# Kernel optimization log

Hardware: AMD Instinct MI355X
Metric: run time of the kernel (lower is better)

The kernel has to match this reference:

```python
import jax, jax.numpy as jnp
import numpy as np

ROI_BATCHSIZE = 512
FG_PER_IMAGE = 128  # round(0.25 * 512)
FG_THRESH = 0.5
BG_HI = 0.5
BG_LO = 0.0


def _make_boxes(key, b, n, img=1024.0):
    k1, k2 = jax.random.split(key)
    xy = jax.random.uniform(k1, (b, n, 2), minval=0.0, maxval=img - 300.0)
    wh = jax.random.uniform(k2, (b, n, 2), minval=8.0, maxval=300.0)
    return jnp.concatenate([xy, xy + wh], axis=-1)  # [b, n, 4] valid x1y1x2y2


def setup_inputs() -> dict:
    key = jax.random.key(0)
    B, R, G = 16, 20000, 100
    k1, k2, k3 = jax.random.split(key, 3)
    roi_boxes = _make_boxes(k1, B, R)
    all_rois = jnp.concatenate([jnp.zeros((B, R, 1), jnp.float32), roi_boxes], axis=-1)
    gt_b = _make_boxes(k2, B, G)
    gt_lab = jax.random.randint(k3, (B, G, 1), 1, 21).astype(jnp.float32)
    gt_boxes = jnp.concatenate([gt_b, gt_lab], axis=-1)
    return {
        "all_rois": all_rois,
        "gt_boxes": gt_boxes,
        "bbox_means": jnp.zeros((4,), jnp.float32),
        "bbox_stds": jnp.array([0.1, 0.1, 0.2, 0.2], jnp.float32),
        "num_gt_boxes": jnp.full((B,), G, jnp.int32),
    }


def _pairwise_iou(a, b):  # a: [B,N,4], b: [B,G,4] -> [B,N,G]
    area_a = (a[..., 2] - a[..., 0] + 1.0) * (a[..., 3] - a[..., 1] + 1.0)
    area_b = (b[..., 2] - b[..., 0] + 1.0) * (b[..., 3] - b[..., 1] + 1.0)
    iw = jnp.clip(jnp.minimum(a[:, :, None, 2], b[:, None, :, 2])
                  - jnp.maximum(a[:, :, None, 0], b[:, None, :, 0]) + 1.0, 0.0)
    ih = jnp.clip(jnp.minimum(a[:, :, None, 3], b[:, None, :, 3])
                  - jnp.maximum(a[:, :, None, 1], b[:, None, :, 1]) + 1.0, 0.0)
    inter = iw * ih
    return inter / (area_a[:, :, None] + area_b[:, None, :] - inter)


def _encode(ex, gt):  # [B,S,4] each -> [B,S,4] (dx, dy, dw, dh)
    ew = ex[..., 2] - ex[..., 0] + 1.0
    eh = ex[..., 3] - ex[..., 1] + 1.0
    ecx = ex[..., 0] + 0.5 * ew
    ecy = ex[..., 1] + 0.5 * eh
    gw = gt[..., 2] - gt[..., 0] + 1.0
    gh = gt[..., 3] - gt[..., 1] + 1.0
    gcx = gt[..., 0] + 0.5 * gw
    gcy = gt[..., 1] + 0.5 * gh
    return jnp.stack([(gcx - ecx) / ew, (gcy - ecy) / eh,
                      jnp.log(gw / ew), jnp.log(gh / eh)], axis=-1)


def _sample_one(key, max_ov, labels_i, rois_i, gta_i, gt_i, img_idx):
    # max_ov: [N]; rois_i: [N,5]; gta_i: [N]; gt_i: [G,5]
    N = max_ov.shape[0]
    S = ROI_BATCHSIZE
    k1, k2, k3, k4 = jax.random.split(key, 4)
    fg = max_ov >= FG_THRESH
    bg = (max_ov < BG_HI) & (max_ov >= BG_LO)
    nfg = fg.sum()
    nbg = bg.sum()
    # random permutation of fg (bg) candidates packed to the front
    fg_order = jnp.argsort(jnp.where(fg, jax.random.uniform(k1, (N,)), 2.0))
    bg_order = jnp.argsort(jnp.where(bg, jax.random.uniform(k2, (N,)), 2.0))
    n_fg_take = jnp.where(nbg > 0, jnp.minimum(FG_PER_IMAGE, nfg), S)
    n_fg_take = jnp.where(nfg > 0, n_fg_take, 0)
    slots = jnp.arange(S)
    rf = jax.random.uniform(k3, (S,))
    rb = jax.random.uniform(k4, (S,))
    # fg without replacement (main path) or with replacement (no-bg path)
    fg_wr = fg_order[jnp.clip((rf * nfg.astype(rf.dtype)).astype(jnp.int32), 0, N - 1)]
    fg_pick = jnp.where(nbg > 0, fg_order[jnp.minimum(slots, N - 1)], fg_wr)
    # bg always sampled with replacement, as in the original
    bg_pick = bg_order[jnp.clip((rb * nbg.astype(rb.dtype)).astype(jnp.int32), 0, N - 1)]
    keep = jnp.where(slots < n_fg_take, fg_pick, bg_pick)  # [S]
    labels = jnp.where(slots < n_fg_take, labels_i[keep], 0.0)
    rois = rois_i[keep].at[:, 0].set(img_idx)
    gt_rois = gt_i[gta_i[keep]]  # [S,5]
    return rois, labels, gt_rois


def _forward(all_rois, gt_boxes, bbox_means, bbox_stds):
    B, G = gt_boxes.shape[0], gt_boxes.shape[1]
    # append gt boxes as rois (col 0 zeroed, cols 1:5 = gt box)
    gt_append = jnp.concatenate(
        [jnp.zeros_like(gt_boxes[..., :1]), gt_boxes[..., :4]], axis=-1)
    all_rois = jnp.concatenate([all_rois, gt_append], axis=1)  # [B, R+G, 5]
    overlaps = _pairwise_iou(all_rois[..., 1:5], gt_boxes[..., :4])  # [B,N,G]
    max_ov = overlaps.max(axis=2)
    gt_assign = overlaps.argmax(axis=2)
    labels = jnp.take_along_axis(gt_boxes[..., 4], gt_assign, axis=1)  # [B,N]
    keys = jax.random.split(jax.random.key(42), B)
    rois_b, labels_b, gt_rois_b = jax.vmap(_sample_one)(
        keys, max_ov, labels, all_rois, gt_assign, gt_boxes,
        jnp.arange(B, dtype=all_rois.dtype))
    targets = _encode(rois_b[..., 1:5], gt_rois_b[..., :4])
    targets = (targets - bbox_means) / bbox_stds
    targets = targets * (labels_b > 0).astype(targets.dtype)[..., None]
    return rois_b, labels_b, targets


def reference(all_rois, gt_boxes, bbox_means, bbox_stds, num_gt_boxes):
    # num_gt_boxes is accepted but unused, as in the original forward
    return _forward(all_rois, gt_boxes, bbox_means, bbox_stds)
```

## Files before the change

kernel.cpp:

```cpp
#include <hip/hip_runtime.h>
#include <stdint.h>


typedef uint32_t u32;
typedef uint64_t u64;

constexpr int B    = 16;
constexpr int R    = 20000;
constexpr int G    = 100;
constexpr int N    = R + G;
constexpr int S    = 512;
constexpr int KFG  = 128;
constexpr int NBKT = 8192;
constexpr u32 SENT = 0xFFFFFFFFu;
constexpr int TPB  = 256;
constexpr int NBLK = (N + TPB - 1) / TPB;

__device__ __forceinline__ void tf2x32(u32 k0, u32 k1, u32 x0, u32 x1,
                                       u32& o0, u32& o1) {
  u32 ks2 = k0 ^ k1 ^ 0x1BD11BDAu;
#define TFR(r) { x0 += x1; x1 = (x1 << (r)) | (x1 >> (32 - (r))); x1 ^= x0; }
  x0 += k0; x1 += k1;
  TFR(13) TFR(15) TFR(26) TFR(6)
  x0 += k1;  x1 += ks2 + 1u;
  TFR(17) TFR(29) TFR(16) TFR(24)
  x0 += ks2; x1 += k0 + 2u;
  TFR(13) TFR(15) TFR(26) TFR(6)
  x0 += k0;  x1 += k1 + 3u;
  TFR(17) TFR(29) TFR(16) TFR(24)
  x0 += k1;  x1 += ks2 + 4u;
  TFR(13) TFR(15) TFR(26) TFR(6)
  x0 += ks2; x1 += k0 + 5u;
#undef TFR
  o0 = x0; o1 = x1;
}

__device__ __forceinline__ void batch_key(int b, u32& kb0, u32& kb1) {
  tf2x32(0u, 42u, 0u, (u32)b, kb0, kb1);
}
__device__ __forceinline__ void sub_key(u32 kb0, u32 kb1, int j, u32& k0, u32& k1) {
  tf2x32(kb0, kb1, 0u, (u32)j, k0, k1);
}
__device__ __forceinline__ u32 rand_bits(u32 k0, u32 k1, int i) {
  u32 b0, b1;
  tf2x32(k0, k1, 0u, (u32)i, b0, b1);
  return b0 ^ b1;
}
__device__ __forceinline__ float bits_to_uniform(u32 bits) {
  return __uint_as_float((bits >> 9) | 0x3f800000u) - 1.0f;
}

__global__ __launch_bounds__(256) void k_zero(uint4* __restrict__ p) {
  const int i = blockIdx.x * 256 + threadIdx.x;
  p[i] = make_uint4(0u, 0u, 0u, 0u);
}

__global__ __launch_bounds__(TPB) void
k_mask(const float* __restrict__ rois, const float* __restrict__ gts,
       u32* __restrict__ fgkey, u32* __restrict__ bgkey,
       u32* __restrict__ cnt,
       u32* __restrict__ minblkF, u32* __restrict__ minblkB) {
#pragma clang fp contract(off)
  __shared__ float4 gbox[G];
  __shared__ float garea[G];
  __shared__ u32 wminF[TPB / 64], wminB[TPB / 64];
  const int b = blockIdx.y;
  if (threadIdx.x < G) {
    const float* gp = gts + (size_t)(b * G + threadIdx.x) * 5;
    float x1 = gp[0], y1 = gp[1], x2 = gp[2], y2 = gp[3];
    gbox[threadIdx.x] = make_float4(x1, y1, x2, y2);
    garea[threadIdx.x] = (x2 - x1 + 1.0f) * (y2 - y1 + 1.0f);
  }
  __syncthreads();

  const int n = blockIdx.x * TPB + threadIdx.x;
  const bool valid = n < N;
  const int nl = valid ? n : 0;

  float ax1, ay1, ax2, ay2;
  if (nl < R) {
    const float* rp = rois + (size_t)(b * R + nl) * 5;
    ax1 = rp[1]; ay1 = rp[2]; ax2 = rp[3]; ay2 = rp[4];
  } else {
    const float* gp = gts + (size_t)(b * G + (nl - R)) * 5;
    ax1 = gp[0]; ay1 = gp[1]; ax2 = gp[2]; ay2 = gp[3];
  }
  const float areaa = (ax2 - ax1 + 1.0f) * (ay2 - ay1 + 1.0f);

  int fg = 0;
#pragma unroll 4
  for (int g = 0; g < G; ++g) {
    const float4 gb = gbox[g];
    const float gar = garea[g];
    float iw = fminf(ax2, gb.z) - fmaxf(ax1, gb.x) + 1.0f;
    iw = fmaxf(iw, 0.0f);
    float ih = fminf(ay2, gb.w) - fmaxf(ay1, gb.y) + 1.0f;
    ih = fmaxf(ih, 0.0f);
    float inter = iw * ih;
    float denom = (areaa + gar) - inter;
    fg |= ((double)inter >= (double)denom * 0x1.ffffffp-2);
  }

  u32 kb0, kb1, k10, k11, k20, k21;
  batch_key(b, kb0, kb1);
  sub_key(kb0, kb1, 0, k10, k11);
  sub_key(kb0, kb1, 1, k20, k21);
  if (valid) {
    u32 u1 = rand_bits(k10, k11, n) >> 9;
    u32 u2 = rand_bits(k20, k21, n) >> 9;
    fgkey[(size_t)b * N + n] = fg ? u1 : SENT;
    bgkey[(size_t)b * N + n] = fg ? SENT : u2;
    const u32 uk = fg ? u1 : u2;
    const int set = fg ? 0 : 1;
    atomicAdd((unsigned int*)&cnt[((size_t)b * 2 + set) * NBKT + (uk >> 10)], 1u);
  }

  u32 vF = (valid && !fg) ? (u32)n : SENT;
  u32 vB = (valid &&  fg) ? (u32)n : SENT;
#pragma unroll
  for (int m = 1; m <= 32; m <<= 1) {
    vF = min(vF, (u32)__shfl_xor((int)vF, m));
    vB = min(vB, (u32)__shfl_xor((int)vB, m));
  }
  if ((threadIdx.x & 63) == 0) {
    wminF[threadIdx.x >> 6] = vF;
    wminB[threadIdx.x >> 6] = vB;
  }
  __syncthreads();
  if (threadIdx.x == 0) {
    u32 mF = SENT, mB = SENT;
#pragma unroll
    for (int w = 0; w < TPB / 64; ++w) { mF = min(mF, wminF[w]); mB = min(mB, wminB[w]); }
    minblkF[b * NBLK + blockIdx.x] = mF;
    minblkB[b * NBLK + blockIdx.x] = mB;
  }
}

__global__ __launch_bounds__(1024) void
k_scan(u32* __restrict__ cnt, u32* __restrict__ cur,
       int* __restrict__ nfg, int* __restrict__ nbg,
       const u32* __restrict__ minblkF, const u32* __restrict__ minblkB,
       u32* __restrict__ slotF, u32* __restrict__ slotB) {
  constexpr int T = 1024;
  constexpr int PER = NBKT / T;
  __shared__ u32 sh[T];
  const int b = blockIdx.x, set = blockIdx.y;
  const int tid = threadIdx.x;
  u32* c = cnt + ((size_t)b * 2 + set) * NBKT;
  u32* q = cur + ((size_t)b * 2 + set) * NBKT;
  u32 local[PER];
  u32 tot = 0;
  const int base = tid * PER;
#pragma unroll
  for (int i = 0; i < PER; ++i) { u32 v = c[base + i]; local[i] = tot; tot += v; }
  sh[tid] = tot;
  __syncthreads();
  for (int off = 1; off < T; off <<= 1) {
    u32 v = (tid >= off) ? sh[tid - off] : 0u;
    __syncthreads();
    sh[tid] += v;
    __syncthreads();
  }
  const u32 pre = sh[tid] - tot;
  const u32 total = sh[T - 1];
#pragma unroll
  for (int i = 0; i < PER; ++i) { u32 v = pre + local[i]; c[base + i] = v; q[base + i] = v; }

  if (tid < 64) {
    const u32* mb = (set ? minblkB : minblkF) + b * NBLK;
    u32 m = SENT;
    for (int i = tid; i < NBLK; i += 64) m = min(m, mb[i]);
#pragma unroll
    for (int mm = 1; mm <= 32; mm <<= 1) m = min(m, (u32)__shfl_xor((int)m, mm));
    if (tid == 0) {
      u32* slot = (set ? slotB : slotF) + (size_t)b * N;
      if (total < (u32)N) slot[total] = (m == SENT) ? 0u : m;
      if (set) nbg[b] = (int)total; else nfg[b] = (int)total;
    }
  }
}

__global__ void k_scatter(const u32* __restrict__ fgkey, const u32* __restrict__ bgkey,
                          u32* __restrict__ cur,
                          u32* __restrict__ slotF, u32* __restrict__ slotB) {
  const int b = blockIdx.y;
  const int n = blockIdx.x * blockDim.x + threadIdx.x;
  if (n >= N) return;
  u32 kf = fgkey[(size_t)b * N + n];
  if (kf != SENT) {
    u32 pos = atomicAdd((unsigned int*)&cur[((size_t)b * 2 + 0) * NBKT + (kf >> 10)], 1u);
    slotF[(size_t)b * N + pos] = ((kf & 1023u) << 15) | (u32)n;
  }
  u32 kb = bgkey[(size_t)b * N + n];
  if (kb != SENT) {
    u32 pos = atomicAdd((unsigned int*)&cur[((size_t)b * 2 + 1) * NBKT + (kb >> 10)], 1u);
    slotB[(size_t)b * N + pos] = ((kb & 1023u) << 15) | (u32)n;
  }
}

__global__ void k_bsort(const u32* __restrict__ cnt ,
                        const u32* __restrict__ cur ,
                        u32* __restrict__ slotF, u32* __restrict__ slotB) {
  const int t = blockIdx.x * blockDim.x + threadIdx.x;
  const int total = B * 2 * NBKT;
  if (t >= total) return;
  const int bs = t / NBKT;
  u32* slot = ((bs & 1) ? slotB : slotF) + (size_t)(bs >> 1) * N;
  const u32 s0 = cnt[t];
  const u32 e = cur[t];
  for (u32 i = s0 + 1; i < e; ++i) {
    u32 v = slot[i];
    int j = (int)i - 1;
    while (j >= (int)s0 && slot[j] > v) { slot[j + 1] = slot[j]; --j; }
    slot[j + 1] = v;
  }
}

__global__ void k_sample(const float* __restrict__ rois, const float* __restrict__ gts,
                         const float* __restrict__ means, const float* __restrict__ stds,
                         const int* __restrict__ nfgA, const int* __restrict__ nbgA,
                         const u32* __restrict__ slotF, const u32* __restrict__ slotB,
                         float* __restrict__ out) {
#pragma clang fp contract(off)
  __shared__ float4 gbox[G];
  __shared__ float garea[G];
  __shared__ float glab[G];
  const int b = blockIdx.x;
  const int s = threadIdx.x;
  if (s < G) {
    const float* gp = gts + (size_t)(b * G + s) * 5;
    float x1 = gp[0], y1 = gp[1], x2 = gp[2], y2 = gp[3];
    gbox[s] = make_float4(x1, y1, x2, y2);
    garea[s] = (x2 - x1 + 1.0f) * (y2 - y1 + 1.0f);
    glab[s] = gp[4];
  }
  __syncthreads();

  const int nfg = nfgA[b];
  const int nbg = nbgA[b];

  u32 kb0, kb1, k30, k31, k40, k41;
  batch_key(b, kb0, kb1);
  sub_key(kb0, kb1, 2, k30, k31);
  sub_key(kb0, kb1, 3, k40, k41);
  float rf = bits_to_uniform(rand_bits(k30, k31, s));
  float rb = bits_to_uniform(rand_bits(k40, k41, s));

  int n_fg_take = (nbg > 0) ? min(KFG, nfg) : S;
  if (nfg <= 0) n_fg_take = 0;

  int keep;
  if (s < n_fg_take) {
    int fi;
    if (nbg > 0) fi = s;
    else {
      fi = (int)(rf * (float)nfg);
      fi = max(0, min(fi, nfg));
    }
    keep = (int)(slotF[(size_t)b * N + fi] & 0x7FFFu);
  } else {
    if (nbg > 0) {
      int bi = (int)(rb * (float)nbg);
      bi = max(0, min(bi, nbg));
      keep = (int)(slotB[(size_t)b * N + bi] & 0x7FFFu);
    } else {
      keep = 0;
    }
  }
  keep = max(0, min(keep, N - 1));

  float ax1, ay1, ax2, ay2;
  if (keep < R) {
    const float* rp = rois + (size_t)(b * R + keep) * 5;
    ax1 = rp[1]; ay1 = rp[2]; ax2 = rp[3]; ay2 = rp[4];
  } else {
    const float4 g2 = gbox[keep - R];
    ax1 = g2.x; ay1 = g2.y; ax2 = g2.z; ay2 = g2.w;
  }
  const float areaa = (ax2 - ax1 + 1.0f) * (ay2 - ay1 + 1.0f);

  float best = -1.0f;
  int arg = 0;
  for (int g = 0; g < G; ++g) {
    const float4 gb = gbox[g];
    const float gar = garea[g];
    float iw = fminf(ax2, gb.z) - fmaxf(ax1, gb.x) + 1.0f;
    iw = fmaxf(iw, 0.0f);
    float ih = fminf(ay2, gb.w) - fmaxf(ay1, gb.y) + 1.0f;
    ih = fmaxf(ih, 0.0f);
    float inter = iw * ih;
    float denom = (areaa + gar) - inter;
    float iou = inter / denom;
    if (iou > best) { best = iou; arg = g; }
  }

  const bool isfg = s < n_fg_take;
  const float label = isfg ? glab[arg] : 0.0f;
  const float4 gbx = gbox[arg];
  const float gx1 = gbx.x, gy1 = gbx.y, gx2 = gbx.z, gy2 = gbx.w;

  float ew = ax2 - ax1 + 1.0f, eh = ay2 - ay1 + 1.0f;
  float ecx = ax1 + 0.5f * ew, ecy = ay1 + 0.5f * eh;
  float gw = gx2 - gx1 + 1.0f, gh = gy2 - gy1 + 1.0f;
  float gcx = gx1 + 0.5f * gw, gcy = gy1 + 0.5f * gh;
  float t0 = (gcx - ecx) / ew;
  float t1 = (gcy - ecy) / eh;
  float t2 = logf(gw / ew);
  float t3 = logf(gh / eh);
  const float msk = (label > 0.0f) ? 1.0f : 0.0f;
  t0 = (t0 - means[0]) / stds[0] * msk;
  t1 = (t1 - means[1]) / stds[1] * msk;
  t2 = (t2 - means[2]) / stds[2] * msk;
  t3 = (t3 - means[3]) / stds[3] * msk;

  float* rout = out;
  float* lout = out + (size_t)B * S * 5;
  float* tout = lout + (size_t)B * S;
  float* rp2 = rout + (size_t)(b * S + s) * 5;
  rp2[0] = (float)b;
  rp2[1] = ax1; rp2[2] = ay1; rp2[3] = ax2; rp2[4] = ay2;
  lout[b * S + s] = label;
  float* tp = tout + (size_t)(b * S + s) * 4;
  tp[0] = t0; tp[1] = t1; tp[2] = t2; tp[3] = t3;
}

extern "C" void kernel_launch(void* const* d_in, const int* in_sizes, int n_in,
                              void* d_out, int out_size, void* d_ws, size_t ws_size,
                              hipStream_t stream) {
  const float* rois  = (const float*)d_in[0];
  const float* gts   = (const float*)d_in[1];
  const float* means = (const float*)d_in[2];
  const float* stds  = (const float*)d_in[3];

  char* ws = (char*)d_ws;
  const size_t per = (size_t)B * N;
  const size_t bkts = (size_t)B * 2 * NBKT;
  u32* fgkey   = (u32*)ws; ws += per * sizeof(u32);
  u32* bgkey   = (u32*)ws; ws += per * sizeof(u32);
  u32* slotF   = (u32*)ws; ws += per * sizeof(u32);
  u32* slotB   = (u32*)ws; ws += per * sizeof(u32);
  u32* cnt     = (u32*)ws; ws += bkts * sizeof(u32);
  u32* cur     = (u32*)ws; ws += bkts * sizeof(u32);
  u32* minblkF = (u32*)ws; ws += (size_t)B * NBLK * sizeof(u32);
  u32* minblkB = (u32*)ws; ws += (size_t)B * NBLK * sizeof(u32);
  int* nfg     = (int*)ws; ws += B * sizeof(int);
  int* nbg     = (int*)ws; ws += B * sizeof(int);

  hipLaunchKernelGGL(k_zero, dim3((int)(bkts / 4 / 256)), dim3(256), 0, stream,
                     (uint4*)cnt);

  hipLaunchKernelGGL(k_mask, dim3(NBLK, B), dim3(TPB), 0, stream,
                     rois, gts, fgkey, bgkey, cnt, minblkF, minblkB);
  hipLaunchKernelGGL(k_scan, dim3(B, 2), dim3(1024), 0, stream,
                     cnt, cur, nfg, nbg, minblkF, minblkB, slotF, slotB);
  hipLaunchKernelGGL(k_scatter, dim3((N + 255) / 256, B), dim3(256), 0, stream,
                     fgkey, bgkey, cur, slotF, slotB);
  hipLaunchKernelGGL(k_bsort, dim3((B * 2 * NBKT + 255) / 256), dim3(256), 0, stream,
                     cnt, cur, slotF, slotB);
  hipLaunchKernelGGL(k_sample, dim3(B), dim3(S), 0, stream,
                     rois, gts, means, stds, nfg, nbg, slotF, slotB,
                     (float*)d_out);
}
```

Measured before the change: 82.35 us.

## Replace per-bucket insertion sort with on-demand rank selection in sampler

```diff
diff --git a/kernel.cpp b/kernel.cpp
--- a/kernel.cpp
+++ b/kernel.cpp
@@ -3,7 +3,6 @@
 
 
 typedef uint32_t u32;
-typedef uint64_t u64;
 
 constexpr int B    = 16;
 constexpr int R    = 20000;
@@ -11,7 +10,7 @@
 constexpr int N    = R + G;
 constexpr int S    = 512;
 constexpr int KFG  = 128;
-constexpr int NBKT = 8192;
+constexpr int NBKT = 2048;
 constexpr u32 SENT = 0xFFFFFFFFu;
 constexpr int TPB  = 256;
 constexpr int NBLK = (N + TPB - 1) / TPB;
@@ -51,14 +50,12 @@
 }
 
 __global__ __launch_bounds__(256) void k_zero(uint4* __restrict__ p) {
-  const int i = blockIdx.x * 256 + threadIdx.x;
-  p[i] = make_uint4(0u, 0u, 0u, 0u);
+  p[blockIdx.x * 256 + threadIdx.x] = make_uint4(0u, 0u, 0u, 0u);
 }
 
 __global__ __launch_bounds__(TPB) void
 k_mask(const float* __restrict__ rois, const float* __restrict__ gts,
-       u32* __restrict__ fgkey, u32* __restrict__ bgkey,
-       u32* __restrict__ cnt,
+       u32* __restrict__ ckey, u32* __restrict__ cnt,
        u32* __restrict__ minblkF, u32* __restrict__ minblkB) {
 #pragma clang fp contract(off)
   __shared__ float4 gbox[G];
@@ -106,13 +103,12 @@
   sub_key(kb0, kb1, 0, k10, k11);
   sub_key(kb0, kb1, 1, k20, k21);
   if (valid) {
-    u32 u1 = rand_bits(k10, k11, n) >> 9;
-    u32 u2 = rand_bits(k20, k21, n) >> 9;
-    fgkey[(size_t)b * N + n] = fg ? u1 : SENT;
-    bgkey[(size_t)b * N + n] = fg ? SENT : u2;
-    const u32 uk = fg ? u1 : u2;
-    const int set = fg ? 0 : 1;
-    atomicAdd((unsigned int*)&cnt[((size_t)b * 2 + set) * NBKT + (uk >> 10)], 1u);
+    u32 kk0 = fg ? k10 : k20;
+    u32 kk1 = fg ? k11 : k21;
+    u32 key = rand_bits(kk0, kk1, n) >> 9;
+    u32 set = fg ? 0u : 1u;
+    ckey[(size_t)b * N + n] = key | (set << 31);
+    atomicAdd((unsigned int*)&cnt[((size_t)b * 2 + set) * NBKT + (key >> 12)], 1u);
   }
 
   u32 vF = (valid && !fg) ? (u32)n : SENT;
@@ -136,103 +132,96 @@
   }
 }
 
-__global__ __launch_bounds__(1024) void
-k_scan(u32* __restrict__ cnt, u32* __restrict__ cur,
+__global__ __launch_bounds__(64) void
+k_scan(u32* __restrict__ cnt,
        int* __restrict__ nfg, int* __restrict__ nbg,
        const u32* __restrict__ minblkF, const u32* __restrict__ minblkB,
        u32* __restrict__ slotF, u32* __restrict__ slotB) {
-  constexpr int T = 1024;
-  constexpr int PER = NBKT / T;
-  __shared__ u32 sh[T];
+  constexpr int PER = NBKT / 64;
   const int b = blockIdx.x, set = blockIdx.y;
-  const int tid = threadIdx.x;
+  const int lane = threadIdx.x;
   u32* c = cnt + ((size_t)b * 2 + set) * NBKT;
-  u32* q = cur + ((size_t)b * 2 + set) * NBKT;
-  u32 local[PER];
+  u32 v[PER];
   u32 tot = 0;
-  const int base = tid * PER;
-#pragma unroll
-  for (int i = 0; i < PER; ++i) { u32 v = c[base + i]; local[i] = tot; tot += v; }
-  sh[tid] = tot;
-  __syncthreads();
-  for (int off = 1; off < T; off <<= 1) {
-    u32 v = (tid >= off) ? sh[tid - off] : 0u;
-    __syncthreads();
-    sh[tid] += v;
-    __syncthreads();
-  }
-  const u32 pre = sh[tid] - tot;
-  const u32 total = sh[T - 1];
-#pragma unroll
-  for (int i = 0; i < PER; ++i) { u32 v = pre + local[i]; c[base + i] = v; q[base + i] = v; }
-
-  if (tid < 64) {
-    const u32* mb = (set ? minblkB : minblkF) + b * NBLK;
-    u32 m = SENT;
-    for (int i = tid; i < NBLK; i += 64) m = min(m, mb[i]);
-#pragma unroll
-    for (int mm = 1; mm <= 32; mm <<= 1) m = min(m, (u32)__shfl_xor((int)m, mm));
-    if (tid == 0) {
-      u32* slot = (set ? slotB : slotF) + (size_t)b * N;
-      if (total < (u32)N) slot[total] = (m == SENT) ? 0u : m;
-      if (set) nbg[b] = (int)total; else nfg[b] = (int)total;
-    }
-  }
-}
-
-__global__ void k_scatter(const u32* __restrict__ fgkey, const u32* __restrict__ bgkey,
-                          u32* __restrict__ cur,
+  const int base = lane * PER;
+#pragma unroll
+  for (int i = 0; i < PER; ++i) { u32 t = c[base + i]; v[i] = tot; tot += t; }
+  u32 run = tot;
+#pragma unroll
+  for (int m = 1; m < 64; m <<= 1) {
+    u32 up = (u32)__shfl_up((int)run, m);
+    if (lane >= m) run += up;
+  }
+  const u32 pre = run - tot;
+  const u32 total = (u32)__shfl((int)run, 63);
+#pragma unroll
+  for (int i = 0; i < PER; ++i) c[base + i] = pre + v[i];
+
+  const u32* mb = (set ? minblkB : minblkF) + b * NBLK;
+  u32 m = SENT;
+  for (int i = lane; i < NBLK; i += 64) m = min(m, mb[i]);
+#pragma unroll
+  for (int mm = 1; mm <= 32; mm <<= 1) m = min(m, (u32)__shfl_xor((int)m, mm));
+  if (lane == 0) {
+    u32* slot = (set ? slotB : slotF) + (size_t)b * N;
+    if (total < (u32)N) slot[total] = (m == SENT) ? 0u : m;
+    if (set) nbg[b] = (int)total; else nfg[b] = (int)total;
+  }
+}
+
+__global__ void k_scatter(const u32* __restrict__ ckey, u32* __restrict__ cnt,
                           u32* __restrict__ slotF, u32* __restrict__ slotB) {
   const int b = blockIdx.y;
   const int n = blockIdx.x * blockDim.x + threadIdx.x;
   if (n >= N) return;
-  u32 kf = fgkey[(size_t)b * N + n];
-  if (kf != SENT) {
-    u32 pos = atomicAdd((unsigned int*)&cur[((size_t)b * 2 + 0) * NBKT + (kf >> 10)], 1u);
-    slotF[(size_t)b * N + pos] = ((kf & 1023u) << 15) | (u32)n;
-  }
-  u32 kb = bgkey[(size_t)b * N + n];
-  if (kb != SENT) {
-    u32 pos = atomicAdd((unsigned int*)&cur[((size_t)b * 2 + 1) * NBKT + (kb >> 10)], 1u);
-    slotB[(size_t)b * N + pos] = ((kb & 1023u) << 15) | (u32)n;
-  }
-}
-
-__global__ void k_bsort(const u32* __restrict__ cnt ,
-                        const u32* __restrict__ cur ,
-                        u32* __restrict__ slotF, u32* __restrict__ slotB) {
-  const int t = blockIdx.x * blockDim.x + threadIdx.x;
-  const int total = B * 2 * NBKT;
-  if (t >= total) return;
-  const int bs = t / NBKT;
-  u32* slot = ((bs & 1) ? slotB : slotF) + (size_t)(bs >> 1) * N;
-  const u32 s0 = cnt[t];
-  const u32 e = cur[t];
-  for (u32 i = s0 + 1; i < e; ++i) {
-    u32 v = slot[i];
-    int j = (int)i - 1;
-    while (j >= (int)s0 && slot[j] > v) { slot[j + 1] = slot[j]; --j; }
-    slot[j + 1] = v;
-  }
-}
-
-__global__ void k_sample(const float* __restrict__ rois, const float* __restrict__ gts,
-                         const float* __restrict__ means, const float* __restrict__ stds,
-                         const int* __restrict__ nfgA, const int* __restrict__ nbgA,
-                         const u32* __restrict__ slotF, const u32* __restrict__ slotB,
-                         float* __restrict__ out) {
+  const u32 w = ckey[(size_t)b * N + n];
+  const u32 set = w >> 31;
+  const u32 key = w & 0x7FFFFFu;
+  u32 pos = atomicAdd((unsigned int*)&cnt[((size_t)b * 2 + set) * NBKT + (key >> 12)], 1u);
+  u32* slot = (set ? slotB : slotF) + (size_t)b * N;
+  slot[pos] = ((key & 4095u) << 15) | (u32)n;
+}
+
+__device__ __forceinline__ int pick_rank(const u32* __restrict__ cend,
+                                         const u32* __restrict__ slot,
+                                         int r, int total) {
+  if (r >= total) return (int)(slot[total] & 0x7FFFu);
+  int lo = 0, hi = NBKT - 1;
+  while (lo < hi) {
+    int mid = (lo + hi) >> 1;
+    if (cend[mid] > (u32)r) hi = mid; else lo = mid + 1;
+  }
+  const u32 bs = lo ? cend[lo - 1] : 0u;
+  const u32 k = cend[lo] - bs;
+  const u32 target = (u32)r - bs;
+  for (u32 i = 0; i < k; ++i) {
+    u32 e = slot[bs + i];
+    u32 rk = 0;
+    for (u32 j = 0; j < k; ++j) rk += (slot[bs + j] < e);
+    if (rk == target) return (int)(e & 0x7FFFu);
+  }
+  return 0;
+}
+
+__global__ __launch_bounds__(128) void
+k_sample(const float* __restrict__ rois, const float* __restrict__ gts,
+         const float* __restrict__ means, const float* __restrict__ stds,
+         const int* __restrict__ nfgA, const int* __restrict__ nbgA,
+         const u32* __restrict__ cnt,
+         const u32* __restrict__ slotF, const u32* __restrict__ slotB,
+         float* __restrict__ out) {
 #pragma clang fp contract(off)
   __shared__ float4 gbox[G];
   __shared__ float garea[G];
   __shared__ float glab[G];
   const int b = blockIdx.x;
-  const int s = threadIdx.x;
-  if (s < G) {
-    const float* gp = gts + (size_t)(b * G + s) * 5;
+  const int s = blockIdx.y * 128 + threadIdx.x;
+  if (threadIdx.x < G) {
+    const float* gp = gts + (size_t)(b * G + threadIdx.x) * 5;
     float x1 = gp[0], y1 = gp[1], x2 = gp[2], y2 = gp[3];
-    gbox[s] = make_float4(x1, y1, x2, y2);
-    garea[s] = (x2 - x1 + 1.0f) * (y2 - y1 + 1.0f);
-    glab[s] = gp[4];
+    gbox[threadIdx.x] = make_float4(x1, y1, x2, y2);
+    garea[threadIdx.x] = (x2 - x1 + 1.0f) * (y2 - y1 + 1.0f);
+    glab[threadIdx.x] = gp[4];
   }
   __syncthreads();
 
@@ -249,23 +238,26 @@
   int n_fg_take = (nbg > 0) ? min(KFG, nfg) : S;
   if (nfg <= 0) n_fg_take = 0;
 
+  const u32* cF = cnt + ((size_t)b * 2 + 0) * NBKT;
+  const u32* cB = cnt + ((size_t)b * 2 + 1) * NBKT;
+  const u32* sF = slotF + (size_t)b * N;
+  const u32* sB = slotB + (size_t)b * N;
+
   int keep;
   if (s < n_fg_take) {
     int fi;
     if (nbg > 0) fi = s;
     else {
       fi = (int)(rf * (float)nfg);
-      fi = max(0, min(fi, nfg));
+      fi = max(0, min(fi, N - 1));
     }
-    keep = (int)(slotF[(size_t)b * N + fi] & 0x7FFFu);
+    keep = pick_rank(cF, sF, fi, nfg);
+  } else if (nbg > 0) {
+    int bi = (int)(rb * (float)nbg);
+    bi = max(0, min(bi, N - 1));
+    keep = pick_rank(cB, sB, bi, nbg);
   } else {
-    if (nbg > 0) {
-      int bi = (int)(rb * (float)nbg);
-      bi = max(0, min(bi, nbg));
-      keep = (int)(slotB[(size_t)b * N + bi] & 0x7FFFu);
-    } else {
-      keep = 0;
-    }
+    keep = 0;
   }
   keep = max(0, min(keep, N - 1));
 
@@ -335,12 +327,10 @@
   char* ws = (char*)d_ws;
   const size_t per = (size_t)B * N;
   const size_t bkts = (size_t)B * 2 * NBKT;
-  u32* fgkey   = (u32*)ws; ws += per * sizeof(u32);
-  u32* bgkey   = (u32*)ws; ws += per * sizeof(u32);
+  u32* ckey    = (u32*)ws; ws += per * sizeof(u32);
   u32* slotF   = (u32*)ws; ws += per * sizeof(u32);
   u32* slotB   = (u32*)ws; ws += per * sizeof(u32);
   u32* cnt     = (u32*)ws; ws += bkts * sizeof(u32);
-  u32* cur     = (u32*)ws; ws += bkts * sizeof(u32);
   u32* minblkF = (u32*)ws; ws += (size_t)B * NBLK * sizeof(u32);
   u32* minblkB = (u32*)ws; ws += (size_t)B * NBLK * sizeof(u32);
   int* nfg     = (int*)ws; ws += B * sizeof(int);
@@ -348,16 +338,13 @@
 
   hipLaunchKernelGGL(k_zero, dim3((int)(bkts / 4 / 256)), dim3(256), 0, stream,
                      (uint4*)cnt);
-
   hipLaunchKernelGGL(k_mask, dim3(NBLK, B), dim3(TPB), 0, stream,
-                     rois, gts, fgkey, bgkey, cnt, minblkF, minblkB);
-  hipLaunchKernelGGL(k_scan, dim3(B, 2), dim3(1024), 0, stream,
-                     cnt, cur, nfg, nbg, minblkF, minblkB, slotF, slotB);
+                     rois, gts, ckey, cnt, minblkF, minblkB);
+  hipLaunchKernelGGL(k_scan, dim3(B, 2), dim3(64), 0, stream,
+                     cnt, nfg, nbg, minblkF, minblkB, slotF, slotB);
   hipLaunchKernelGGL(k_scatter, dim3((N + 255) / 256, B), dim3(256), 0, stream,
-                     fgkey, bgkey, cur, slotF, slotB);
-  hipLaunchKernelGGL(k_bsort, dim3((B * 2 * NBKT + 255) / 256), dim3(256), 0, stream,
-                     cnt, cur, slotF, slotB);
-  hipLaunchKernelGGL(k_sample, dim3(B), dim3(S), 0, stream,
-                     rois, gts, means, stds, nfg, nbg, slotF, slotB,
+                     ckey, cnt, slotF, slotB);
+  hipLaunchKernelGGL(k_sample, dim3(B, S / 128), dim3(128), 0, stream,
+                     rois, gts, means, stds, nfg, nbg, cnt, slotF, slotB,
                      (float*)d_out);
 }
```

Result: slower. 95.26 us (+15.7%).

## Merge fg/bg key arrays, shrink bucket count, split sampling across blocks

Applied to the files above, without the earlier changes.

```diff
diff --git a/kernel.cpp b/kernel.cpp
--- a/kernel.cpp
+++ b/kernel.cpp
@@ -3,7 +3,6 @@
 
 
 typedef uint32_t u32;
-typedef uint64_t u64;
 
 constexpr int B    = 16;
 constexpr int R    = 20000;
@@ -11,7 +10,7 @@
 constexpr int N    = R + G;
 constexpr int S    = 512;
 constexpr int KFG  = 128;
-constexpr int NBKT = 8192;
+constexpr int NBKT = 2048;
 constexpr u32 SENT = 0xFFFFFFFFu;
 constexpr int TPB  = 256;
 constexpr int NBLK = (N + TPB - 1) / TPB;
@@ -51,14 +50,12 @@
 }
 
 __global__ __launch_bounds__(256) void k_zero(uint4* __restrict__ p) {
-  const int i = blockIdx.x * 256 + threadIdx.x;
-  p[i] = make_uint4(0u, 0u, 0u, 0u);
+  p[blockIdx.x * 256 + threadIdx.x] = make_uint4(0u, 0u, 0u, 0u);
 }
 
 __global__ __launch_bounds__(TPB) void
 k_mask(const float* __restrict__ rois, const float* __restrict__ gts,
-       u32* __restrict__ fgkey, u32* __restrict__ bgkey,
-       u32* __restrict__ cnt,
+       u32* __restrict__ ckey, u32* __restrict__ cnt,
        u32* __restrict__ minblkF, u32* __restrict__ minblkB) {
 #pragma clang fp contract(off)
   __shared__ float4 gbox[G];
@@ -106,13 +103,12 @@
   sub_key(kb0, kb1, 0, k10, k11);
   sub_key(kb0, kb1, 1, k20, k21);
   if (valid) {
-    u32 u1 = rand_bits(k10, k11, n) >> 9;
-    u32 u2 = rand_bits(k20, k21, n) >> 9;
-    fgkey[(size_t)b * N + n] = fg ? u1 : SENT;
-    bgkey[(size_t)b * N + n] = fg ? SENT : u2;
-    const u32 uk = fg ? u1 : u2;
-    const int set = fg ? 0 : 1;
-    atomicAdd((unsigned int*)&cnt[((size_t)b * 2 + set) * NBKT + (uk >> 10)], 1u);
+    u32 kk0 = fg ? k10 : k20;
+    u32 kk1 = fg ? k11 : k21;
+    u32 key = rand_bits(kk0, kk1, n) >> 9;
+    u32 set = fg ? 0u : 1u;
+    ckey[(size_t)b * N + n] = key | (set << 31);
+    atomicAdd((unsigned int*)&cnt[((size_t)b * 2 + set) * NBKT + (key >> 12)], 1u);
   }
 
   u32 vF = (valid && !fg) ? (u32)n : SENT;
@@ -180,22 +176,17 @@
   }
 }
 
-__global__ void k_scatter(const u32* __restrict__ fgkey, const u32* __restrict__ bgkey,
-                          u32* __restrict__ cur,
+__global__ void k_scatter(const u32* __restrict__ ckey, u32* __restrict__ cur,
                           u32* __restrict__ slotF, u32* __restrict__ slotB) {
   const int b = blockIdx.y;
   const int n = blockIdx.x * blockDim.x + threadIdx.x;
   if (n >= N) return;
-  u32 kf = fgkey[(size_t)b * N + n];
-  if (kf != SENT) {
-    u32 pos = atomicAdd((unsigned int*)&cur[((size_t)b * 2 + 0) * NBKT + (kf >> 10)], 1u);
-    slotF[(size_t)b * N + pos] = ((kf & 1023u) << 15) | (u32)n;
-  }
-  u32 kb = bgkey[(size_t)b * N + n];
-  if (kb != SENT) {
-    u32 pos = atomicAdd((unsigned int*)&cur[((size_t)b * 2 + 1) * NBKT + (kb >> 10)], 1u);
-    slotB[(size_t)b * N + pos] = ((kb & 1023u) << 15) | (u32)n;
-  }
+  const u32 w = ckey[(size_t)b * N + n];
+  const u32 set = w >> 31;
+  const u32 key = w & 0x7FFFFFu;
+  u32 pos = atomicAdd((unsigned int*)&cur[((size_t)b * 2 + set) * NBKT + (key >> 12)], 1u);
+  u32* slot = (set ? slotB : slotF) + (size_t)b * N;
+  slot[pos] = ((key & 4095u) << 15) | (u32)n;
 }
 
 __global__ void k_bsort(const u32* __restrict__ cnt ,
@@ -216,23 +207,24 @@
   }
 }
 
-__global__ void k_sample(const float* __restrict__ rois, const float* __restrict__ gts,
-                         const float* __restrict__ means, const float* __restrict__ stds,
-                         const int* __restrict__ nfgA, const int* __restrict__ nbgA,
-                         const u32* __restrict__ slotF, const u32* __restrict__ slotB,
-                         float* __restrict__ out) {
+__global__ __launch_bounds__(128) void
+k_sample(const float* __restrict__ rois, const float* __restrict__ gts,
+         const float* __restrict__ means, const float* __restrict__ stds,
+         const int* __restrict__ nfgA, const int* __restrict__ nbgA,
+         const u32* __restrict__ slotF, const u32* __restrict__ slotB,
+         float* __restrict__ out) {
 #pragma clang fp contract(off)
   __shared__ float4 gbox[G];
   __shared__ float garea[G];
   __shared__ float glab[G];
   const int b = blockIdx.x;
-  const int s = threadIdx.x;
-  if (s < G) {
-    const float* gp = gts + (size_t)(b * G + s) * 5;
+  const int s = blockIdx.y * 128 + threadIdx.x;
+  if (threadIdx.x < G) {
+    const float* gp = gts + (size_t)(b * G + threadIdx.x) * 5;
     float x1 = gp[0], y1 = gp[1], x2 = gp[2], y2 = gp[3];
-    gbox[s] = make_float4(x1, y1, x2, y2);
-    garea[s] = (x2 - x1 + 1.0f) * (y2 - y1 + 1.0f);
-    glab[s] = gp[4];
+    gbox[threadIdx.x] = make_float4(x1, y1, x2, y2);
+    garea[threadIdx.x] = (x2 - x1 + 1.0f) * (y2 - y1 + 1.0f);
+    glab[threadIdx.x] = gp[4];
   }
   __syncthreads();
 
@@ -335,8 +327,7 @@
   char* ws = (char*)d_ws;
   const size_t per = (size_t)B * N;
   const size_t bkts = (size_t)B * 2 * NBKT;
-  u32* fgkey   = (u32*)ws; ws += per * sizeof(u32);
-  u32* bgkey   = (u32*)ws; ws += per * sizeof(u32);
+  u32* ckey    = (u32*)ws; ws += per * sizeof(u32);
   u32* slotF   = (u32*)ws; ws += per * sizeof(u32);
   u32* slotB   = (u32*)ws; ws += per * sizeof(u32);
   u32* cnt     = (u32*)ws; ws += bkts * sizeof(u32);
@@ -348,16 +339,15 @@
 
   hipLaunchKernelGGL(k_zero, dim3((int)(bkts / 4 / 256)), dim3(256), 0, stream,
                      (uint4*)cnt);
-
   hipLaunchKernelGGL(k_mask, dim3(NBLK, B), dim3(TPB), 0, stream,
-                     rois, gts, fgkey, bgkey, cnt, minblkF, minblkB);
+                     rois, gts, ckey, cnt, minblkF, minblkB);
   hipLaunchKernelGGL(k_scan, dim3(B, 2), dim3(1024), 0, stream,
                      cnt, cur, nfg, nbg, minblkF, minblkB, slotF, slotB);
   hipLaunchKernelGGL(k_scatter, dim3((N + 255) / 256, B), dim3(256), 0, stream,
-                     fgkey, bgkey, cur, slotF, slotB);
+                     ckey, cur, slotF, slotB);
   hipLaunchKernelGGL(k_bsort, dim3((B * 2 * NBKT + 255) / 256), dim3(256), 0, stream,
                      cnt, cur, slotF, slotB);
-  hipLaunchKernelGGL(k_sample, dim3(B), dim3(S), 0, stream,
+  hipLaunchKernelGGL(k_sample, dim3(B, S / 128), dim3(128), 0, stream,
                      rois, gts, means, stds, nfg, nbg, slotF, slotB,
                      (float*)d_out);
 }
```

New measurement: 105.7 us. +28.3%, slower.
